# Performance work log

Measured on AMD Instinct MI355X. Metric: run time of the kernel, lower is better.

The kernel has to match this reference:

```python
import jax, jax.numpy as jnp
import numpy as np

B, E, C = 1024, 512, 16384
MRG, ALPHA, V, K, LAM, TAU = 0.1, 32.0, 100.0, 1.0, 0.1, 1.5


def _l2norm(x):
    # matches torch l2_norm: divide by sqrt(sum(x^2) + 1e-12) row-wise
    n = jnp.sqrt(jnp.sum(x * x, axis=1) + 1e-12)
    return x / n[:, None]


def setup_inputs() -> dict:
    key = jax.random.key(0)
    k1, k2, k3, k4, k5 = jax.random.split(key, 5)
    inputsBatch = _l2norm(jax.random.normal(k1, (B, E), dtype=jnp.float32))
    targetsBatch = jax.random.randint(k2, (B,), 0, C, dtype=jnp.int32)
    # kaiming_normal fan_out on (C, E): std = sqrt(2 / E)
    proxies = jax.random.normal(k3, (C, E), dtype=jnp.float32) * np.sqrt(2.0 / E).astype(np.float32)
    effectiveNum = jax.random.uniform(k4, (C,), dtype=jnp.float32) * 100.0
    learnedSim = jax.random.uniform(k5, (C,), dtype=jnp.float32)
    return {"inputsBatch": inputsBatch, "targetsBatch": targetsBatch,
            "proxies": proxies, "effectiveNum": effectiveNum, "learnedSim": learnedSim}


def reference(inputsBatch, targetsBatch, proxies, effectiveNum, learnedSim):
    nb_classes = proxies.shape[0]
    P = jax.nn.one_hot(targetsBatch, nb_classes, dtype=inputsBatch.dtype)  # [B, C]
    N = 1.0 - P
    proxy_l2 = _l2norm(proxies)
    cos = inputsBatch @ proxy_l2.T  # [B, C]

    classCnt = P.sum(axis=0)                      # [C]
    present = (classCnt > 0).astype(cos.dtype)

    w_base = 1.0 / (1.0 + jnp.log1p(effectiveNum))
    eta = (1.0 + K * (1.0 - learnedSim)) * w_base + LAM
    outlierSim = learnedSim - eta                 # [C]

    # enableFilter=False: mask at positive positions stays 1, so each present
    # class contributes mean(ones)=1 to pos_weight_sum
    pos_weight_sum = jnp.sum(present)

    # negative-position adaptive reweighting (vectorized over the class loop)
    neg_vals = jnp.where(cos < outlierSim[None, :],
                         (1.0 / jnp.maximum(1.0, effectiveNum))[None, :],
                         1.0)                      # [B, C]
    Ncnt = N.sum(axis=0)
    neg_mean = jnp.sum(N * neg_vals, axis=0) / jnp.maximum(Ncnt, 1.0)
    neg_weight_sum = jnp.sum(jnp.where(Ncnt > 0, neg_mean, 0.0))

    mask = jnp.where(N > 0, neg_vals, 1.0)        # 1 at positive entries

    pos_term = jnp.sum(jnp.log1p(jnp.sum(P * jnp.exp(ALPHA * (MRG - cos) * mask), axis=0)))
    neg_term = jnp.sum(jnp.log1p(jnp.sum(N * jnp.exp(ALPHA * (cos + MRG) * mask), axis=0)))

    return pos_term / pos_weight_sum + neg_term / neg_weight_sum
```

## Files before the change

### kernel.cpp

```cpp
#include <hip/hip_runtime.h>
#include <math.h>

#define B_SZ 1024
#define E_SZ 512
#define C_SZ 16384
#define MRG 0.1f
#define ALPHA 32.0f
#define K_HY 1.0f
#define LAM 0.1f

typedef __bf16 bf16;
typedef bf16 bf16x8 __attribute__((ext_vector_type(8)));
typedef float f32x4 __attribute__((ext_vector_type(4)));

__device__ __forceinline__ void async16(const void* g, void* l) {
    __builtin_amdgcn_global_load_lds(
        (const __attribute__((address_space(1))) void*)g,
        (__attribute__((address_space(3))) void*)l,
        16, 0, 0);
}

__global__ __launch_bounds__(256) void prologue(
    const float* __restrict__ proxies, bf16* __restrict__ Pbf,
    const float* __restrict__ effNum, const float* __restrict__ lSim,
    const float* __restrict__ x, bf16* __restrict__ Abf,
    float* __restrict__ oSim, float* __restrict__ iEff,
    float* __restrict__ posExp, float* __restrict__ negExp,
    float* __restrict__ negVals, int* __restrict__ posCnt,
    float* __restrict__ acc4, int* __restrict__ ticket) {
    if (blockIdx.x < 4096) {
        int row = (blockIdx.x * 256 + threadIdx.x) >> 6;
        int lane = threadIdx.x & 63;
        const float* pr = proxies + (size_t)row * E_SZ + lane * 8;
        float4 v0 = *(const float4*)pr;
        float4 v1 = *(const float4*)(pr + 4);
        float ss = v0.x * v0.x + v0.y * v0.y + v0.z * v0.z + v0.w * v0.w +
                   v1.x * v1.x + v1.y * v1.y + v1.z * v1.z + v1.w * v1.w;
#pragma unroll
        for (int m = 1; m < 64; m <<= 1) ss += __shfl_xor(ss, m);
        float inv = 1.0f / sqrtf(ss + 1e-12f);
        bf16x8 o;
        o[0] = (bf16)(v0.x * inv); o[1] = (bf16)(v0.y * inv);
        o[2] = (bf16)(v0.z * inv); o[3] = (bf16)(v0.w * inv);
        o[4] = (bf16)(v1.x * inv); o[5] = (bf16)(v1.y * inv);
        o[6] = (bf16)(v1.z * inv); o[7] = (bf16)(v1.w * inv);
        *(bf16x8*)(Pbf + (size_t)row * E_SZ + lane * 8) = o;
    } else {
        int t = (blockIdx.x - 4096) * 256 + threadIdx.x;
        size_t f0 = (size_t)t * 8;
        float4 v0 = *(const float4*)(x + f0);
        float4 v1 = *(const float4*)(x + f0 + 4);
        bf16x8 o;
        o[0] = (bf16)v0.x; o[1] = (bf16)v0.y; o[2] = (bf16)v0.z; o[3] = (bf16)v0.w;
        o[4] = (bf16)v1.x; o[5] = (bf16)v1.y; o[6] = (bf16)v1.z; o[7] = (bf16)v1.w;
        *(bf16x8*)(Abf + f0) = o;
        if (t < C_SZ) {
            float en = effNum[t], ls = lSim[t];
            float wb = 1.0f / (1.0f + log1pf(en));
            float eta = (1.0f + K_HY * (1.0f - ls)) * wb + LAM;
            oSim[t] = ls - eta;
            iEff[t] = 1.0f / fmaxf(1.0f, en);
            posExp[t] = 0.f; negExp[t] = 0.f; negVals[t] = 0.f; posCnt[t] = 0;
            if (t < 8) acc4[t] = 0.f;
            if (t == 8) ticket[0] = 0;
        }
    }
}

__global__ __launch_bounds__(256) void gemm_epilogue(
    const bf16* __restrict__ Abf,
    const bf16* __restrict__ Pbf,
    const int* __restrict__ targets,
    const float* __restrict__ oSimA,
    const float* __restrict__ iEffA,
    float* __restrict__ posExp,
    float* __restrict__ negExp,
    float* __restrict__ negVals,
    int* __restrict__ posCnt) {
    __shared__ __align__(16) bf16 Alds[2][128 * 32];
    __shared__ __align__(16) bf16 Blds[2][128 * 32];
    __shared__ int tgtLds[128];

    const int tid = threadIdx.x;
    const int wave = tid >> 6, lane = tid & 63;
    const int quad = lane >> 4, l16 = lane & 15;
    const int wRow = (wave >> 1) * 64, wCol = (wave & 1) * 64;
    const int bn0 = blockIdx.x * 128, bm0 = blockIdx.y * 128;

    if (tid < 128) tgtLds[tid] = targets[bm0 + tid];

    const bf16* gA = Abf + (size_t)(bm0 + wave * 32 + l16) * E_SZ + quad * 8;
    const bf16* gB = Pbf + (size_t)(bn0 + wave * 32 + l16) * E_SZ + quad * 8;

    int colG[4]; float oS[4], iE[4];
#pragma unroll
    for (int ni = 0; ni < 4; ++ni) {
        colG[ni] = bn0 + wCol + ni * 16 + l16;
        oS[ni] = oSimA[colG[ni]];
        iE[ni] = iEffA[colG[ni]];
    }

    f32x4 zero = {0.f, 0.f, 0.f, 0.f};
    f32x4 acc[4][4];
#pragma unroll
    for (int i = 0; i < 4; ++i)
#pragma unroll
        for (int j = 0; j < 4; ++j) acc[i][j] = zero;

#define STAGE(K0, BUF)                                                           \
    {                                                                            \
        _Pragma("unroll")                                                        \
        for (int j = 0; j < 2; ++j) {                                            \
            int chunk = wave * 2 + j;                                            \
            async16(gA + (size_t)j * 16 * E_SZ + (K0), &Alds[BUF][chunk * 512]); \
            async16(gB + (size_t)j * 16 * E_SZ + (K0), &Blds[BUF][chunk * 512]); \
        }                                                                        \
    }

    STAGE(0, 0)
#pragma unroll
    for (int kk = 0; kk < 16; ++kk) {
        __syncthreads();
        if (kk < 15) STAGE((kk + 1) * 32, (kk + 1) & 1)
        const int bsel = kk & 1;
        bf16x8 af[4], bff[4];
#pragma unroll
        for (int mi = 0; mi < 4; ++mi)
            af[mi] = *(const bf16x8*)&Alds[bsel][((wRow >> 4) + mi) * 512 + quad * 128 + l16 * 8];
#pragma unroll
        for (int ni = 0; ni < 4; ++ni)
            bff[ni] = *(const bf16x8*)&Blds[bsel][((wCol >> 4) + ni) * 512 + quad * 128 + l16 * 8];
#pragma unroll
        for (int mi = 0; mi < 4; ++mi)
#pragma unroll
            for (int ni = 0; ni < 4; ++ni)
                acc[mi][ni] = __builtin_amdgcn_mfma_f32_16x16x32_bf16(
                    af[mi], bff[ni], acc[mi][ni], 0, 0, 0);
    }
#undef STAGE

    float negE[4] = {0.f, 0.f, 0.f, 0.f};
    float negV[4] = {0.f, 0.f, 0.f, 0.f};
#pragma unroll
    for (int mi = 0; mi < 4; ++mi) {
#pragma unroll
        for (int r = 0; r < 4; ++r) {
            int rowL = wRow + mi * 16 + quad * 4 + r;
            int tgt = tgtLds[rowL];
#pragma unroll
            for (int ni = 0; ni < 4; ++ni) {
                float cosv = acc[mi][ni][r];
                if (tgt == colG[ni]) {
                    atomicAdd(&posExp[colG[ni]], __expf(ALPHA * (MRG - cosv)));
                    atomicAdd(&posCnt[colG[ni]], 1);
                } else {
                    float nv = (cosv < oS[ni]) ? iE[ni] : 1.0f;
                    negE[ni] += __expf(ALPHA * (cosv + MRG) * nv);
                    negV[ni] += nv;
                }
            }
        }
    }
#pragma unroll
    for (int ni = 0; ni < 4; ++ni) {
        float e = negE[ni], v = negV[ni];
        e += __shfl_xor(e, 16); e += __shfl_xor(e, 32);
        v += __shfl_xor(v, 16); v += __shfl_xor(v, 32);
        if (quad == 0) {
            atomicAdd(&negExp[colG[ni]], e);
            atomicAdd(&negVals[colG[ni]], v);
        }
    }
}

__global__ __launch_bounds__(256) void finalize(
    const float* __restrict__ posExp, const float* __restrict__ negExp,
    const float* __restrict__ negVals, const int* __restrict__ posCnt,
    float* __restrict__ acc4, int* __restrict__ ticket,
    float* __restrict__ out) {
    int tid = threadIdx.x;
    int c = blockIdx.x * 256 + tid;
    float pt = log1pf(posExp[c]);
    float nt = log1pf(negExp[c]);
    int cnt = posCnt[c];
    float pws = (cnt > 0) ? 1.0f : 0.0f;
    int Nc = B_SZ - cnt;
    float nws = (Nc > 0) ? negVals[c] / (float)Nc : 0.0f;
#pragma unroll
    for (int m = 1; m < 64; m <<= 1) {
        pt += __shfl_xor(pt, m);
        nt += __shfl_xor(nt, m);
        pws += __shfl_xor(pws, m);
        nws += __shfl_xor(nws, m);
    }
    __shared__ float red[4][4];
    int wv = tid >> 6;
    if ((tid & 63) == 0) {
        red[wv][0] = pt; red[wv][1] = nt; red[wv][2] = pws; red[wv][3] = nws;
    }
    __syncthreads();
    if (tid < 4) {
        float s = red[0][tid] + red[1][tid] + red[2][tid] + red[3][tid];
        atomicAdd(&acc4[tid], s);
    }
    __syncthreads();
    if (tid == 0) {
        __threadfence();
        int old = atomicAdd(ticket, 1);
        if (old == 63) {
            float a0 = atomicAdd(&acc4[0], 0.f);
            float a1 = atomicAdd(&acc4[1], 0.f);
            float a2 = atomicAdd(&acc4[2], 0.f);
            float a3 = atomicAdd(&acc4[3], 0.f);
            out[0] = a0 / a2 + a1 / a3;
        }
    }
}

extern "C" void kernel_launch(void* const* d_in, const int* in_sizes, int n_in,
                              void* d_out, int out_size, void* d_ws, size_t ws_size,
                              hipStream_t stream) {
    const float* inputs = (const float*)d_in[0];
    const int* targets = (const int*)d_in[1];
    const float* proxies = (const float*)d_in[2];
    const float* effNum = (const float*)d_in[3];
    const float* lSim = (const float*)d_in[4];
    float* out = (float*)d_out;

    bf16* Pbf = (bf16*)d_ws;
    bf16* Abf = Pbf + (size_t)C_SZ * E_SZ;
    float* oSim = (float*)(Abf + (size_t)B_SZ * E_SZ);
    float* iEff = oSim + C_SZ;
    float* posExp = iEff + C_SZ;
    float* negExp = posExp + C_SZ;
    float* negVals = negExp + C_SZ;
    int* posCnt = (int*)(negVals + C_SZ);
    float* acc4 = (float*)(posCnt + C_SZ);
    int* ticket = (int*)(acc4 + 8);

    prologue<<<4096 + 256, 256, 0, stream>>>(proxies, Pbf, effNum, lSim, inputs,
                                             Abf, oSim, iEff, posExp, negExp,
                                             negVals, posCnt, acc4, ticket);
    gemm_epilogue<<<dim3(C_SZ / 128, B_SZ / 128), 256, 0, stream>>>(
        Abf, Pbf, targets, oSim, iEff, posExp, negExp, negVals, posCnt);
    finalize<<<C_SZ / 256, 256, 0, stream>>>(posExp, negExp, negVals, posCnt,
                                             acc4, ticket, out);
}
```

Measured before the change: 137.9 us.

## Shrink GEMM tile to 64x128 and fuse finalize into GEMM via ticket barrier

The GEMM tile shrinks from 128x128 to 64x128, which doubles the grid to 2048 blocks for better occupancy and load balance across CUs, and the A/B staging is merged into one shared buffer. The separate finalize kernel is removed. The last 64 blocks to finish take a ticket, spin on a flag set by the final block, then do the per-class reduction and write the output. This saves a kernel launch but relies on spin-waiting blocks being co-resident, and the smaller tile lowers data reuse per block.

Measured after the change: 259.8 us. +88.5%, slower.

```diff
diff --git a/kernel.cpp b/kernel.cpp
--- a/kernel.cpp
+++ b/kernel.cpp
@@ -9,6 +9,9 @@
 #define K_HY 1.0f
 #define LAM 0.1f
 
+#define NBLK 2048
+#define NFIN 64
+
 typedef __bf16 bf16;
 typedef bf16 bf16x8 __attribute__((ext_vector_type(8)));
 typedef float f32x4 __attribute__((ext_vector_type(4)));
@@ -27,7 +30,7 @@
     float* __restrict__ oSim, float* __restrict__ iEff,
     float* __restrict__ posExp, float* __restrict__ negExp,
     float* __restrict__ negVals, int* __restrict__ posCnt,
-    float* __restrict__ acc4, int* __restrict__ ticket) {
+    float* __restrict__ acc4, int* __restrict__ ctrl) {
     if (blockIdx.x < 4096) {
         int row = (blockIdx.x * 256 + threadIdx.x) >> 6;
         int lane = threadIdx.x & 63;
@@ -62,7 +65,7 @@
             iEff[t] = 1.0f / fmaxf(1.0f, en);
             posExp[t] = 0.f; negExp[t] = 0.f; negVals[t] = 0.f; posCnt[t] = 0;
             if (t < 8) acc4[t] = 0.f;
-            if (t == 8) ticket[0] = 0;
+            if (t < 3) ctrl[t] = 0;
         }
     }
 }
@@ -76,21 +79,31 @@
     float* __restrict__ posExp,
     float* __restrict__ negExp,
     float* __restrict__ negVals,
-    int* __restrict__ posCnt) {
-    __shared__ __align__(16) bf16 Alds[2][128 * 32];
-    __shared__ __align__(16) bf16 Blds[2][128 * 32];
-    __shared__ int tgtLds[128];
+    int* __restrict__ posCnt,
+    float* __restrict__ acc4,
+    int* __restrict__ ctrl,
+    float* __restrict__ out) {
+    __shared__ __align__(16) bf16 S[2][12 * 512];
+    __shared__ int tgtLds[64];
+    __shared__ int tkt;
+    __shared__ float red[4][4];
 
     const int tid = threadIdx.x;
     const int wave = tid >> 6, lane = tid & 63;
     const int quad = lane >> 4, l16 = lane & 15;
-    const int wRow = (wave >> 1) * 64, wCol = (wave & 1) * 64;
-    const int bn0 = blockIdx.x * 128, bm0 = blockIdx.y * 128;
-
-    if (tid < 128) tgtLds[tid] = targets[bm0 + tid];
-
-    const bf16* gA = Abf + (size_t)(bm0 + wave * 32 + l16) * E_SZ + quad * 8;
-    const bf16* gB = Pbf + (size_t)(bn0 + wave * 32 + l16) * E_SZ + quad * 8;
+    const int wRow = (wave >> 1) * 32, wCol = (wave & 1) * 64;
+    const int bn0 = blockIdx.x * 128, bm0 = blockIdx.y * 64;
+
+    if (tid < 64) tgtLds[tid] = targets[bm0 + tid];
+
+    const bf16* srcs[3];
+#pragma unroll
+    for (int j = 0; j < 3; ++j) {
+        int c = wave * 3 + j;
+        srcs[j] = (c < 4)
+            ? Abf + (size_t)(bm0 + c * 16 + l16) * E_SZ + quad * 8
+            : Pbf + (size_t)(bn0 + (c - 4) * 16 + l16) * E_SZ + quad * 8;
+    }
 
     int colG[4]; float oS[4], iE[4];
 #pragma unroll
@@ -101,20 +114,17 @@
     }
 
     f32x4 zero = {0.f, 0.f, 0.f, 0.f};
-    f32x4 acc[4][4];
-#pragma unroll
-    for (int i = 0; i < 4; ++i)
+    f32x4 acc[2][4];
+#pragma unroll
+    for (int i = 0; i < 2; ++i)
 #pragma unroll
         for (int j = 0; j < 4; ++j) acc[i][j] = zero;
 
-#define STAGE(K0, BUF)                                                           \
-    {                                                                            \
-        _Pragma("unroll")                                                        \
-        for (int j = 0; j < 2; ++j) {                                            \
-            int chunk = wave * 2 + j;                                            \
-            async16(gA + (size_t)j * 16 * E_SZ + (K0), &Alds[BUF][chunk * 512]); \
-            async16(gB + (size_t)j * 16 * E_SZ + (K0), &Blds[BUF][chunk * 512]); \
-        }                                                                        \
+#define STAGE(K0, BUF)                                                   \
+    {                                                                    \
+        _Pragma("unroll")                                                \
+        for (int j = 0; j < 3; ++j)                                      \
+            async16(srcs[j] + (K0), &S[BUF][(wave * 3 + j) * 512]);      \
     }
 
     STAGE(0, 0)
@@ -123,15 +133,15 @@
         __syncthreads();
         if (kk < 15) STAGE((kk + 1) * 32, (kk + 1) & 1)
         const int bsel = kk & 1;
-        bf16x8 af[4], bff[4];
-#pragma unroll
-        for (int mi = 0; mi < 4; ++mi)
-            af[mi] = *(const bf16x8*)&Alds[bsel][((wRow >> 4) + mi) * 512 + quad * 128 + l16 * 8];
+        bf16x8 af[2], bff[4];
+#pragma unroll
+        for (int mi = 0; mi < 2; ++mi)
+            af[mi] = *(const bf16x8*)&S[bsel][((wRow >> 4) + mi) * 512 + quad * 128 + l16 * 8];
 #pragma unroll
         for (int ni = 0; ni < 4; ++ni)
-            bff[ni] = *(const bf16x8*)&Blds[bsel][((wCol >> 4) + ni) * 512 + quad * 128 + l16 * 8];
-#pragma unroll
-        for (int mi = 0; mi < 4; ++mi)
+            bff[ni] = *(const bf16x8*)&S[bsel][2048 + ((wCol >> 4) + ni) * 512 + quad * 128 + l16 * 8];
+#pragma unroll
+        for (int mi = 0; mi < 2; ++mi)
 #pragma unroll
             for (int ni = 0; ni < 4; ++ni)
                 acc[mi][ni] = __builtin_amdgcn_mfma_f32_16x16x32_bf16(
@@ -142,7 +152,7 @@
     float negE[4] = {0.f, 0.f, 0.f, 0.f};
     float negV[4] = {0.f, 0.f, 0.f, 0.f};
 #pragma unroll
-    for (int mi = 0; mi < 4; ++mi) {
+    for (int mi = 0; mi < 2; ++mi) {
 #pragma unroll
         for (int r = 0; r < 4; ++r) {
             int rowL = wRow + mi * 16 + quad * 4 + r;
@@ -171,21 +181,35 @@
             atomicAdd(&negVals[colG[ni]], v);
         }
     }
-}
-
-__global__ __launch_bounds__(256) void finalize(
-    const float* __restrict__ posExp, const float* __restrict__ negExp,
-    const float* __restrict__ negVals, const int* __restrict__ posCnt,
-    float* __restrict__ acc4, int* __restrict__ ticket,
-    float* __restrict__ out) {
-    int tid = threadIdx.x;
-    int c = blockIdx.x * 256 + tid;
-    float pt = log1pf(posExp[c]);
-    float nt = log1pf(negExp[c]);
-    int cnt = posCnt[c];
+
+    int* ticket = ctrl;
+    int* flag = ctrl + 1;
+    int* ticket2 = ctrl + 2;
+    __threadfence();
+    if (tid == 0) tkt = atomicAdd(ticket, 1);
+    __syncthreads();
+    int t = tkt;
+    if (t < NBLK - NFIN) return;
+    int fb = t - (NBLK - NFIN);
+    if (tid == 0) {
+        if (t == NBLK - 1)
+            __hip_atomic_store(flag, 1, __ATOMIC_RELEASE, __HIP_MEMORY_SCOPE_AGENT);
+        while (__hip_atomic_load(flag, __ATOMIC_ACQUIRE, __HIP_MEMORY_SCOPE_AGENT) == 0)
+            __builtin_amdgcn_s_sleep(8);
+    }
+    __syncthreads();
+    __threadfence();
+
+    int c = fb * 256 + tid;
+    float pe = __hip_atomic_load(&posExp[c], __ATOMIC_RELAXED, __HIP_MEMORY_SCOPE_AGENT);
+    float ne = __hip_atomic_load(&negExp[c], __ATOMIC_RELAXED, __HIP_MEMORY_SCOPE_AGENT);
+    float nv = __hip_atomic_load(&negVals[c], __ATOMIC_RELAXED, __HIP_MEMORY_SCOPE_AGENT);
+    int cnt = __hip_atomic_load(&posCnt[c], __ATOMIC_RELAXED, __HIP_MEMORY_SCOPE_AGENT);
+    float pt = log1pf(pe);
+    float nt = log1pf(ne);
     float pws = (cnt > 0) ? 1.0f : 0.0f;
     int Nc = B_SZ - cnt;
-    float nws = (Nc > 0) ? negVals[c] / (float)Nc : 0.0f;
+    float nws = (Nc > 0) ? nv / (float)Nc : 0.0f;
 #pragma unroll
     for (int m = 1; m < 64; m <<= 1) {
         pt += __shfl_xor(pt, m);
@@ -193,10 +217,8 @@
         pws += __shfl_xor(pws, m);
         nws += __shfl_xor(nws, m);
     }
-    __shared__ float red[4][4];
-    int wv = tid >> 6;
     if ((tid & 63) == 0) {
-        red[wv][0] = pt; red[wv][1] = nt; red[wv][2] = pws; red[wv][3] = nws;
+        red[wave][0] = pt; red[wave][1] = nt; red[wave][2] = pws; red[wave][3] = nws;
     }
     __syncthreads();
     if (tid < 4) {
@@ -206,8 +228,7 @@
     __syncthreads();
     if (tid == 0) {
         __threadfence();
-        int old = atomicAdd(ticket, 1);
-        if (old == 63) {
+        if (atomicAdd(ticket2, 1) == NFIN - 1) {
             float a0 = atomicAdd(&acc4[0], 0.f);
             float a1 = atomicAdd(&acc4[1], 0.f);
             float a2 = atomicAdd(&acc4[2], 0.f);
@@ -236,13 +257,12 @@
     float* negVals = negExp + C_SZ;
     int* posCnt = (int*)(negVals + C_SZ);
     float* acc4 = (float*)(posCnt + C_SZ);
-    int* ticket = (int*)(acc4 + 8);
+    int* ctrl = (int*)(acc4 + 8);
 
     prologue<<<4096 + 256, 256, 0, stream>>>(proxies, Pbf, effNum, lSim, inputs,
                                              Abf, oSim, iEff, posExp, negExp,
-                                             negVals, posCnt, acc4, ticket);
-    gemm_epilogue<<<dim3(C_SZ / 128, B_SZ / 128), 256, 0, stream>>>(
-        Abf, Pbf, targets, oSim, iEff, posExp, negExp, negVals, posCnt);
-    finalize<<<C_SZ / 256, 256, 0, stream>>>(posExp, negExp, negVals, posCnt,
-                                             acc4, ticket, out);
-}
+                                             negVals, posCnt, acc4, ctrl);
+    gemm_epilogue<<<dim3(C_SZ / 128, B_SZ / 64), 256, 0, stream>>>(
+        Abf, Pbf, targets, oSim, iEff, posExp, negExp, negVals, posCnt,
+        acc4, ctrl, out);
+}
```
